# Kernel optimization log

Measured on AMD Instinct MI355X. Metric: run time of the kernel, lower is better.

Reference implementation:

```python
import jax, jax.numpy as jnp
import numpy as np

N_QUBITS = 15
N_LAYERS = 4
N_GATES = 3   # gate_pool = [rx, ry, rz]
N_CLASSES = 4
K_PRIME = 4
BATCH = 64
TAU = 1.0


def _gate_bank(theta):
    """theta: float[...]. Returns complex64[..., 3, 2, 2] = stacked RX/RY/RZ(theta)."""
    th = theta.astype(jnp.float32)
    c = jnp.cos(th / 2).astype(jnp.complex64)
    s = jnp.sin(th / 2).astype(jnp.complex64)
    z = jnp.zeros_like(c)
    isn = 1j * s
    rx = jnp.stack([jnp.stack([c, -isn], -1), jnp.stack([-isn, c], -1)], -2)
    ry = jnp.stack([jnp.stack([c, -s], -1), jnp.stack([s, c], -1)], -2)
    e_m = jnp.exp(-0.5j * th).astype(jnp.complex64)
    e_p = jnp.exp(0.5j * th).astype(jnp.complex64)
    rz = jnp.stack([jnp.stack([e_m, z], -1), jnp.stack([z, e_p], -1)], -2)
    return jnp.stack([rx, ry, rz], -3)


def _apply_1q(state, U, q):
    """Apply a single-qubit gate to qubit q. state: [B] + [2]*n. U: [2,2] or [B,2,2]."""
    s = jnp.moveaxis(state, 1 + q, -1)
    if U.ndim == 2:
        s = jnp.einsum('ij,b...j->b...i', U, s)
    else:
        s = jnp.einsum('bij,b...j->b...i', U, s)
    return jnp.moveaxis(s, -1, 1 + q)


def _apply_cnot(state, c, t):
    """CNOT with control c, target t on state [B] + [2]*n."""
    c0 = jax.lax.slice_in_dim(state, 0, 1, axis=1 + c)
    c1 = jax.lax.slice_in_dim(state, 1, 2, axis=1 + c)
    c1 = jnp.flip(c1, axis=1 + t)
    return jnp.concatenate([c0, c1], axis=1 + c)


def setup_inputs() -> dict:
    key = jax.random.key(0)
    k1, k2, k3, k4, k5 = jax.random.split(key, 5)
    x = jax.random.uniform(k1, (BATCH, N_QUBITS), jnp.float32) * np.float32(np.pi)
    P = jax.random.normal(k2, (N_LAYERS, N_QUBITS, 1, K_PRIME), jnp.float32)
    Q = jax.random.normal(k3, (N_LAYERS, N_QUBITS, K_PRIME, N_GATES), jnp.float32)
    rotation_params = jax.random.uniform(k4, (N_LAYERS * N_QUBITS,), jnp.float32) * np.float32(2 * np.pi)
    u = jax.random.uniform(k5, (N_LAYERS, N_QUBITS, N_GATES), jnp.float32, 1e-6, 1.0 - 1e-6)
    gumbel_noise = -jnp.log(-jnp.log(u))
    return {"x": x, "P": P, "Q": Q, "rotation_params": rotation_params,
            "gumbel_noise": gumbel_noise}


def reference(x, P, Q, rotation_params, gumbel_noise):
    B = x.shape[0]
    n = N_QUBITS
    # architecture logits = (P @ Q).squeeze(2)  -> [L, n, G]
    logits = (P @ Q).squeeze(2)
    # hard gumbel-softmax with straight-through estimator
    y_soft = jax.nn.softmax((logits + gumbel_noise) / TAU, axis=-1)
    y_hard = jax.nn.one_hot(jnp.argmax(y_soft, axis=-1), N_GATES, dtype=y_soft.dtype)
    onehot = y_hard + y_soft - jax.lax.stop_gradient(y_soft)  # [L, n, G]

    # |0...0> initial state, shape [B] + [2]*n
    state = jnp.zeros((B,) + (2,) * n, jnp.complex64).at[(slice(None),) + (0,) * n].set(1.0)

    # angle-encode data: RY(x_q) on qubit q
    enc = _gate_bank(x)[..., 1, :, :]  # [B, n, 2, 2] (RY bank)
    for q in range(n):
        state = _apply_1q(state, enc[:, q], q)

    # per-layer selected parametrized rotations, mixed by one-hot (hard fwd, soft grad)
    theta = rotation_params.reshape(N_LAYERS, n)
    banks = _gate_bank(theta)  # [L, n, 3, 2, 2]
    U = jnp.einsum('lqg,lqgij->lqij', onehot.astype(jnp.complex64), banks)
    for l in range(N_LAYERS):
        for q in range(n):
            state = _apply_1q(state, U[l, q], q)
        for q in range(n):  # entangling CNOT ring
            state = _apply_cnot(state, q, (q + 1) % n)

    amps = state.reshape(B, -1)
    probs = amps.real ** 2 + amps.imag ** 2  # [B, 2^n]
    M = probs.shape[1]
    # aggregate contiguous basis-state blocks into class probabilities
    return probs.reshape(B, N_CLASSES, M // N_CLASSES).sum(-1)
```

## Files before the change

### kernel.cpp

```cpp
#include <hip/hip_runtime.h>

#define BLOCK 512
#define NAMPS 64
#define CHUNK 32

struct St {
  float2 a0,a1,a2,a3,a4,a5,a6,a7,a8,a9,a10,a11,a12,a13,a14,a15,
         a16,a17,a18,a19,a20,a21,a22,a23,a24,a25,a26,a27,a28,a29,a30,a31,
         a32,a33,a34,a35,a36,a37,a38,a39,a40,a41,a42,a43,a44,a45,a46,a47,
         a48,a49,a50,a51,a52,a53,a54,a55,a56,a57,a58,a59,a60,a61,a62,a63;
  template<int I> __device__ __forceinline__ float2& g(){
    if constexpr (I==0) return a0;   else if constexpr (I==1) return a1;
    else if constexpr (I==2) return a2;   else if constexpr (I==3) return a3;
    else if constexpr (I==4) return a4;   else if constexpr (I==5) return a5;
    else if constexpr (I==6) return a6;   else if constexpr (I==7) return a7;
    else if constexpr (I==8) return a8;   else if constexpr (I==9) return a9;
    else if constexpr (I==10) return a10; else if constexpr (I==11) return a11;
    else if constexpr (I==12) return a12; else if constexpr (I==13) return a13;
    else if constexpr (I==14) return a14; else if constexpr (I==15) return a15;
    else if constexpr (I==16) return a16; else if constexpr (I==17) return a17;
    else if constexpr (I==18) return a18; else if constexpr (I==19) return a19;
    else if constexpr (I==20) return a20; else if constexpr (I==21) return a21;
    else if constexpr (I==22) return a22; else if constexpr (I==23) return a23;
    else if constexpr (I==24) return a24; else if constexpr (I==25) return a25;
    else if constexpr (I==26) return a26; else if constexpr (I==27) return a27;
    else if constexpr (I==28) return a28; else if constexpr (I==29) return a29;
    else if constexpr (I==30) return a30; else if constexpr (I==31) return a31;
    else if constexpr (I==32) return a32; else if constexpr (I==33) return a33;
    else if constexpr (I==34) return a34; else if constexpr (I==35) return a35;
    else if constexpr (I==36) return a36; else if constexpr (I==37) return a37;
    else if constexpr (I==38) return a38; else if constexpr (I==39) return a39;
    else if constexpr (I==40) return a40; else if constexpr (I==41) return a41;
    else if constexpr (I==42) return a42; else if constexpr (I==43) return a43;
    else if constexpr (I==44) return a44; else if constexpr (I==45) return a45;
    else if constexpr (I==46) return a46; else if constexpr (I==47) return a47;
    else if constexpr (I==48) return a48; else if constexpr (I==49) return a49;
    else if constexpr (I==50) return a50; else if constexpr (I==51) return a51;
    else if constexpr (I==52) return a52; else if constexpr (I==53) return a53;
    else if constexpr (I==54) return a54; else if constexpr (I==55) return a55;
    else if constexpr (I==56) return a56; else if constexpr (I==57) return a57;
    else if constexpr (I==58) return a58; else if constexpr (I==59) return a59;
    else if constexpr (I==60) return a60; else if constexpr (I==61) return a61;
    else if constexpr (I==62) return a62; else return a63;
  }
};

__device__ __forceinline__ float2 cmadd2(float2 u, float2 a, float2 v, float2 b){
  return make_float2(u.x*a.x - u.y*a.y + v.x*b.x - v.y*b.y,
                     u.x*a.y + u.y*a.x + v.x*b.y + v.y*b.x);
}


template<int BL, int K>
__device__ __forceinline__ void rot_local_impl(St& st, float2 u00, float2 u01, float2 u10, float2 u11){
  if constexpr (K < NAMPS){
    if constexpr (!(K & (1<<BL))){
      constexpr int K1 = K | (1<<BL);
      float2 x0 = st.g<K>(), x1 = st.g<K1>();
      st.g<K>()  = cmadd2(u00, x0, u01, x1);
      st.g<K1>() = cmadd2(u10, x0, u11, x1);
    }
    rot_local_impl<BL, K+1>(st, u00, u01, u10, u11);
  }
}
template<int BL>
__device__ __forceinline__ void rot_local(St& st, const float* u){
  float2 u00 = make_float2(u[0],u[1]), u01 = make_float2(u[2],u[3]);
  float2 u10 = make_float2(u[4],u[5]), u11 = make_float2(u[6],u[7]);
  rot_local_impl<BL, 0>(st, u00, u01, u10, u11);
}

template<int LB, int K>
__device__ __forceinline__ void rot_lane_impl(St& st, float2 ua, float2 ub){
  if constexpr (K < NAMPS){
    float2 A = st.g<K>();
    float2 p;
    p.x = __shfl_xor(A.x, 1<<LB, 64);
    p.y = __shfl_xor(A.y, 1<<LB, 64);
    st.g<K>() = cmadd2(ua, A, ub, p);
    rot_lane_impl<LB, K+1>(st, ua, ub);
  }
}
template<int LB>
__device__ __forceinline__ void rot_lane(St& st, const float* u, int lane){
  const int bit = (lane >> LB) & 1;
  float2 u00 = make_float2(u[0],u[1]), u01 = make_float2(u[2],u[3]);
  float2 u10 = make_float2(u[4],u[5]), u11 = make_float2(u[6],u[7]);
  float2 ua = bit ? u11 : u00;
  float2 ub = bit ? u10 : u01;
  rot_lane_impl<LB, 0>(st, ua, ub);
}

template<int Base, int K>
__device__ __forceinline__ void stw_impl(St& st, float2* xbuf, int t){
  if constexpr (K < CHUNK){
    xbuf[K*BLOCK + t] = st.g<Base + K>();
    stw_impl<Base, K+1>(st, xbuf, t);
  }
}
template<int Base, int K>
__device__ __forceinline__ void ldr_rot_impl(St& st, const float2* xbuf, int partner, float2 ua, float2 ub){
  if constexpr (K < CHUNK){
    float2 p = xbuf[K*BLOCK + partner];
    float2 A = st.g<Base + K>();
    st.g<Base + K>() = cmadd2(ua, A, ub, p);
    ldr_rot_impl<Base, K+1>(st, xbuf, partner, ua, ub);
  }
}
template<int Base, int K>
__device__ __forceinline__ void ldr_mov_impl(St& st, const float2* xbuf, int src){
  if constexpr (K < CHUNK){
    st.g<Base + K>() = xbuf[K*BLOCK + src];
    ldr_mov_impl<Base, K+1>(st, xbuf, src);
  }
}

template<int WB>
__device__ __forceinline__ void rot_wave(St& st, const float* u, int t, float2* xbuf){
  const int partner = t ^ (64 << WB);
  const int bit = (t >> (6 + WB)) & 1;
  float2 u00 = make_float2(u[0],u[1]), u01 = make_float2(u[2],u[3]);
  float2 u10 = make_float2(u[4],u[5]), u11 = make_float2(u[6],u[7]);
  float2 ua = bit ? u11 : u00;
  float2 ub = bit ? u10 : u01;
  __syncthreads();
  stw_impl<0, 0>(st, xbuf, t);
  __syncthreads();
  ldr_rot_impl<0, 0>(st, xbuf, partner, ua, ub);
  __syncthreads();
  stw_impl<32, 0>(st, xbuf, t);
  __syncthreads();
  ldr_rot_impl<32, 0>(st, xbuf, partner, ua, ub);
}

__device__ __forceinline__ void cnot_wavechain(St& st, int t, float2* xbuf){
  const int wave = t >> 6, lane = t & 63;
  const int src = ((wave ^ ((wave >> 1) & 3)) << 6) | lane;
  __syncthreads();
  stw_impl<0, 0>(st, xbuf, t);
  __syncthreads();
  ldr_mov_impl<0, 0>(st, xbuf, src);
  __syncthreads();
  stw_impl<32, 0>(st, xbuf, t);
  __syncthreads();
  ldr_mov_impl<32, 0>(st, xbuf, src);
}

template<int K>
__device__ __forceinline__ void lanechain_impl(St& st, int src){
  if constexpr (K < NAMPS){
    float2 A = st.g<K>();
    float2 p;
    p.x = __shfl(A.x, src, 64);
    p.y = __shfl(A.y, src, 64);
    st.g<K>() = p;
    lanechain_impl<K+1>(st, src);
  }
}
__device__ __forceinline__ void cnot_lanechain(St& st, int t){
  const int lane = t & 63;
  const int w0 = (t >> 6) & 1;
  const int src = lane ^ ((lane >> 1) & 31) ^ (w0 << 5);
  lanechain_impl<0>(st, src);
}

template<int K>
__device__ __forceinline__ void q8_impl(St& st, bool ctrl){
  if constexpr (K < 32){
    constexpr int K1 = K | 32;
    float2 x0 = st.g<K>(), x1 = st.g<K1>();
    st.g<K>()  = ctrl ? x1 : x0;
    st.g<K1>() = ctrl ? x0 : x1;
    q8_impl<K+1>(st, ctrl);
  }
}

template<int K>
__device__ __forceinline__ void ripple_impl(St& dst, St& src){
  if constexpr (K < NAMPS){
    dst.g<K>() = src.g<K ^ ((K>>1) & 31)>();
    ripple_impl<K+1>(dst, src);
  }
}

template<int K>
__device__ __forceinline__ void q14_w_impl(St& st, float2* xbuf, int t){
  if constexpr (K < 32){
    xbuf[K*BLOCK + t] = st.g<2*K + 1>();
    q14_w_impl<K+1>(st, xbuf, t);
  }
}
template<int K>
__device__ __forceinline__ void q14_r_impl(St& st, const float2* xbuf, int partner){
  if constexpr (K < 32){
    st.g<2*K + 1>() = xbuf[K*BLOCK + partner];
    q14_r_impl<K+1>(st, xbuf, partner);
  }
}
__device__ __forceinline__ void cnot_q14(St& st, int t, float2* xbuf){
  const int partner = t ^ 256;
  __syncthreads();
  q14_w_impl<0>(st, xbuf, t);
  __syncthreads();
  q14_r_impl<0>(st, xbuf, partner);
}

template<int K>
__device__ __forceinline__ void init_impl(St& st, float hp,
                                          float lc0, float lc1, float lc2, float lc3, float lc4, float lc5,
                                          float ls0, float ls1, float ls2, float ls3, float ls4, float ls5){
  if constexpr (K < NAMPS){
    float v = hp;
    v *= (K & 32) ? ls5 : lc5;
    v *= (K & 16) ? ls4 : lc4;
    v *= (K & 8)  ? ls3 : lc3;
    v *= (K & 4)  ? ls2 : lc2;
    v *= (K & 2)  ? ls1 : lc1;
    v *= (K & 1)  ? ls0 : lc0;
    st.g<K>() = make_float2(v, 0.f);
    init_impl<K+1>(st, hp, lc0,lc1,lc2,lc3,lc4,lc5, ls0,ls1,ls2,ls3,ls4,ls5);
  }
}

template<int K>
__device__ __forceinline__ float sumsq_impl(St& st, float acc){
  if constexpr (K < NAMPS){
    float2 A = st.g<K>();
    return sumsq_impl<K+1>(st, acc + A.x*A.x + A.y*A.y);
  } else return acc;
}

__global__ __attribute__((amdgpu_flat_work_group_size(BLOCK,BLOCK), amdgpu_waves_per_eu(2,2)))
void qdarts_kernel(const float* __restrict__ x,
                   const float* __restrict__ P,
                   const float* __restrict__ Q,
                   const float* __restrict__ rot,
                   const float* __restrict__ gn,
                   float* __restrict__ out)
{
  __shared__ float2 xbuf[CHUNK * BLOCK];
  __shared__ float  umat[60 * 8];
  __shared__ float  part[8];

  const int t    = threadIdx.x;
  const int b    = blockIdx.x;
  const int lane = t & 63;
  const int wave = t >> 6;

  if (t < 60){
    const int idx = t;
    const float* Pv = P  + idx*4;
    const float* Qv = Q  + idx*12;
    const float* gv = gn + idx*3;
    int g = 0; float best = -1e30f;
    #pragma unroll
    for (int j = 0; j < 3; j++){
      float lg = Pv[0]*Qv[0*3+j] + Pv[1]*Qv[1*3+j] + Pv[2]*Qv[2*3+j] + Pv[3]*Qv[3*3+j] + gv[j];
      if (lg > best){ best = lg; g = j; }
    }
    const float half = rot[idx] * 0.5f;
    const float c = cosf(half), s = sinf(half);
    float m0,m1,m2,m3,m4,m5,m6,m7;
    if (g == 0){
      m0=c; m1=0.f; m2=0.f; m3=-s; m4=0.f; m5=-s; m6=c; m7=0.f;
    } else if (g == 1){
      m0=c; m1=0.f; m2=-s; m3=0.f; m4=s; m5=0.f; m6=c; m7=0.f;
    } else {
      m0=c; m1=-s; m2=0.f; m3=0.f; m4=0.f; m5=0.f; m6=c; m7=s;
    }
    umat[idx*8+0]=m0; umat[idx*8+1]=m1; umat[idx*8+2]=m2; umat[idx*8+3]=m3;
    umat[idx*8+4]=m4; umat[idx*8+5]=m5; umat[idx*8+6]=m6; umat[idx*8+7]=m7;
  }
  __syncthreads();

  const float* xb = x + b*15;
  float hp = 1.f;
  #pragma unroll
  for (int q = 0; q < 9; q++){
    const float h = xb[q]*0.5f;
    hp *= ((t >> (8-q)) & 1) ? sinf(h) : cosf(h);
  }
  float lc0,lc1,lc2,lc3,lc4,lc5, ls0,ls1,ls2,ls3,ls4,ls5;
  { float h;
    h = xb[14]*0.5f; lc0 = cosf(h); ls0 = sinf(h);
    h = xb[13]*0.5f; lc1 = cosf(h); ls1 = sinf(h);
    h = xb[12]*0.5f; lc2 = cosf(h); ls2 = sinf(h);
    h = xb[11]*0.5f; lc3 = cosf(h); ls3 = sinf(h);
    h = xb[10]*0.5f; lc4 = cosf(h); ls4 = sinf(h);
    h = xb[9] *0.5f; lc5 = cosf(h); ls5 = sinf(h);
  }
  St st;
  init_impl<0>(st, hp, lc0,lc1,lc2,lc3,lc4,lc5, ls0,ls1,ls2,ls3,ls4,ls5);

  for (int l = 0; l < 4; l++){
    const float* U = umat + l*15*8;
    rot_local<5>(st, U + 9*8);
    rot_local<4>(st, U + 10*8);
    rot_local<3>(st, U + 11*8);
    rot_local<2>(st, U + 12*8);
    rot_local<1>(st, U + 13*8);
    rot_local<0>(st, U + 14*8);
    rot_lane<5>(st, U + 3*8, lane);
    rot_lane<4>(st, U + 4*8, lane);
    rot_lane<3>(st, U + 5*8, lane);
    rot_lane<2>(st, U + 6*8, lane);
    rot_lane<1>(st, U + 7*8, lane);
    rot_lane<0>(st, U + 8*8, lane);
    rot_wave<2>(st, U + 0*8, t, xbuf);
    rot_wave<1>(st, U + 1*8, t, xbuf);
    rot_wave<0>(st, U + 2*8, t, xbuf);
    cnot_wavechain(st, t, xbuf);
    cnot_lanechain(st, t);
    q8_impl<0>(st, (bool)(lane & 1));
    { St tmp; ripple_impl<0>(tmp, st); st = tmp; }
    cnot_q14(st, t, xbuf);
  }

  float s = sumsq_impl<0>(st, 0.f);
  #pragma unroll
  for (int off = 32; off > 0; off >>= 1) s += __shfl_down(s, off, 64);
  if (lane == 0) part[wave] = s;
  __syncthreads();
  if (t < 4){
    out[b*4 + t] = part[2*t] + part[2*t+1];
  }
}

extern "C" void kernel_launch(void* const* d_in, const int* in_sizes, int n_in,
                              void* d_out, int out_size, void* d_ws, size_t ws_size,
                              hipStream_t stream) {
  const float* x   = (const float*)d_in[0];
  const float* P   = (const float*)d_in[1];
  const float* Q   = (const float*)d_in[2];
  const float* rot = (const float*)d_in[3];
  const float* gn  = (const float*)d_in[4];
  float* out = (float*)d_out;
  hipLaunchKernelGGL(qdarts_kernel, dim3(64), dim3(BLOCK), 0, stream,
                     x, P, Q, rot, gn, out);
}
```

Measured before the change: 225.8 us.

## Use DPP for low-lane rotations, 128-bit LDS exchanges, fuse q2 rotation with CNOT chain

Measured after the change: 237.6 us. +5.2%, slower.

```diff
diff --git a/kernel.cpp b/kernel.cpp
--- a/kernel.cpp
+++ b/kernel.cpp
@@ -91,32 +91,61 @@
   rot_lane_impl<LB, 0>(st, ua, ub);
 }
 
-template<int Base, int K>
-__device__ __forceinline__ void stw_impl(St& st, float2* xbuf, int t){
-  if constexpr (K < CHUNK){
-    xbuf[K*BLOCK + t] = st.g<Base + K>();
-    stw_impl<Base, K+1>(st, xbuf, t);
-  }
-}
-template<int Base, int K>
-__device__ __forceinline__ void ldr_rot_impl(St& st, const float2* xbuf, int partner, float2 ua, float2 ub){
-  if constexpr (K < CHUNK){
-    float2 p = xbuf[K*BLOCK + partner];
-    float2 A = st.g<Base + K>();
-    st.g<Base + K>() = cmadd2(ua, A, ub, p);
-    ldr_rot_impl<Base, K+1>(st, xbuf, partner, ua, ub);
-  }
-}
-template<int Base, int K>
-__device__ __forceinline__ void ldr_mov_impl(St& st, const float2* xbuf, int src){
-  if constexpr (K < CHUNK){
-    st.g<Base + K>() = xbuf[K*BLOCK + src];
-    ldr_mov_impl<Base, K+1>(st, xbuf, src);
+template<int CTRL>
+__device__ __forceinline__ float dppf(float v){
+  int i = __float_as_int(v);
+  return __int_as_float(__builtin_amdgcn_update_dpp(i, i, CTRL, 0xF, 0xF, false));
+}
+template<int CTRL, int K>
+__device__ __forceinline__ void rot_dpp_impl(St& st, float2 ua, float2 ub){
+  if constexpr (K < NAMPS){
+    float2 A = st.g<K>();
+    float2 p = make_float2(dppf<CTRL>(A.x), dppf<CTRL>(A.y));
+    st.g<K>() = cmadd2(ua, A, ub, p);
+    rot_dpp_impl<CTRL, K+1>(st, ua, ub);
+  }
+}
+template<int LB, int CTRL>
+__device__ __forceinline__ void rot_dpp(St& st, const float* u, int lane){
+  const int bit = (lane >> LB) & 1;
+  float2 u00 = make_float2(u[0],u[1]), u01 = make_float2(u[2],u[3]);
+  float2 u10 = make_float2(u[4],u[5]), u11 = make_float2(u[6],u[7]);
+  float2 ua = bit ? u11 : u00;
+  float2 ub = bit ? u10 : u01;
+  rot_dpp_impl<CTRL, 0>(st, ua, ub);
+}
+
+template<int Base, int K2>
+__device__ __forceinline__ void stw128_impl(St& st, float4* xb4, int t){
+  if constexpr (K2 < 16){
+    float2 a = st.g<Base + 2*K2>(), b = st.g<Base + 2*K2 + 1>();
+    xb4[K2*BLOCK + t] = make_float4(a.x, a.y, b.x, b.y);
+    stw128_impl<Base, K2+1>(st, xb4, t);
+  }
+}
+template<int Base, int K2>
+__device__ __forceinline__ void ldr128_rot_impl(St& st, const float4* xb4, int partner, float2 ua, float2 ub){
+  if constexpr (K2 < 16){
+    float4 p = xb4[K2*BLOCK + partner];
+    float2 A = st.g<Base + 2*K2>(), B = st.g<Base + 2*K2 + 1>();
+    st.g<Base + 2*K2>()     = cmadd2(ua, A, ub, make_float2(p.x, p.y));
+    st.g<Base + 2*K2 + 1>() = cmadd2(ua, B, ub, make_float2(p.z, p.w));
+    ldr128_rot_impl<Base, K2+1>(st, xb4, partner, ua, ub);
+  }
+}
+template<int Base, int K2>
+__device__ __forceinline__ void fread_impl(St& st, const float4* xb4, int s, int s2, float2 ua, float2 ub){
+  if constexpr (K2 < 16){
+    float4 p = xb4[K2*BLOCK + s];
+    float4 q = xb4[K2*BLOCK + s2];
+    st.g<Base + 2*K2>()     = cmadd2(ua, make_float2(p.x,p.y), ub, make_float2(q.x,q.y));
+    st.g<Base + 2*K2 + 1>() = cmadd2(ua, make_float2(p.z,p.w), ub, make_float2(q.z,q.w));
+    fread_impl<Base, K2+1>(st, xb4, s, s2, ua, ub);
   }
 }
 
 template<int WB>
-__device__ __forceinline__ void rot_wave(St& st, const float* u, int t, float2* xbuf){
+__device__ __forceinline__ void rot_wave(St& st, const float* u, int t, float4* xb4){
   const int partner = t ^ (64 << WB);
   const int bit = (t >> (6 + WB)) & 1;
   float2 u00 = make_float2(u[0],u[1]), u01 = make_float2(u[2],u[3]);
@@ -124,26 +153,32 @@
   float2 ua = bit ? u11 : u00;
   float2 ub = bit ? u10 : u01;
   __syncthreads();
-  stw_impl<0, 0>(st, xbuf, t);
-  __syncthreads();
-  ldr_rot_impl<0, 0>(st, xbuf, partner, ua, ub);
-  __syncthreads();
-  stw_impl<32, 0>(st, xbuf, t);
-  __syncthreads();
-  ldr_rot_impl<32, 0>(st, xbuf, partner, ua, ub);
-}
-
-__device__ __forceinline__ void cnot_wavechain(St& st, int t, float2* xbuf){
+  stw128_impl<0, 0>(st, xb4, t);
+  __syncthreads();
+  ldr128_rot_impl<0, 0>(st, xb4, partner, ua, ub);
+  __syncthreads();
+  stw128_impl<32, 0>(st, xb4, t);
+  __syncthreads();
+  ldr128_rot_impl<32, 0>(st, xb4, partner, ua, ub);
+}
+
+__device__ __forceinline__ void rotq2_wavechain(St& st, const float* u, int t, float4* xb4){
   const int wave = t >> 6, lane = t & 63;
-  const int src = ((wave ^ ((wave >> 1) & 3)) << 6) | lane;
-  __syncthreads();
-  stw_impl<0, 0>(st, xbuf, t);
-  __syncthreads();
-  ldr_mov_impl<0, 0>(st, xbuf, src);
-  __syncthreads();
-  stw_impl<32, 0>(st, xbuf, t);
-  __syncthreads();
-  ldr_mov_impl<32, 0>(st, xbuf, src);
+  const int s  = ((wave ^ ((wave >> 1) & 3)) << 6) | lane;
+  const int s2 = s ^ 64;
+  const int sbit = (s >> 6) & 1;
+  float2 u00 = make_float2(u[0],u[1]), u01 = make_float2(u[2],u[3]);
+  float2 u10 = make_float2(u[4],u[5]), u11 = make_float2(u[6],u[7]);
+  float2 ua = sbit ? u11 : u00;
+  float2 ub = sbit ? u10 : u01;
+  __syncthreads();
+  stw128_impl<0, 0>(st, xb4, t);
+  __syncthreads();
+  fread_impl<0, 0>(st, xb4, s, s2, ua, ub);
+  __syncthreads();
+  stw128_impl<32, 0>(st, xb4, t);
+  __syncthreads();
+  fread_impl<32, 0>(st, xb4, s, s2, ua, ub);
 }
 
 template<int K>
@@ -184,25 +219,25 @@
 }
 
 template<int K>
-__device__ __forceinline__ void q14_w_impl(St& st, float2* xbuf, int t){
+__device__ __forceinline__ void q14_w_impl(St& st, float2* xb2, int t){
   if constexpr (K < 32){
-    xbuf[K*BLOCK + t] = st.g<2*K + 1>();
-    q14_w_impl<K+1>(st, xbuf, t);
-  }
-}
-template<int K>
-__device__ __forceinline__ void q14_r_impl(St& st, const float2* xbuf, int partner){
+    xb2[K*BLOCK + t] = st.g<2*K + 1>();
+    q14_w_impl<K+1>(st, xb2, t);
+  }
+}
+template<int K>
+__device__ __forceinline__ void q14_r_impl(St& st, const float2* xb2, int partner){
   if constexpr (K < 32){
-    st.g<2*K + 1>() = xbuf[K*BLOCK + partner];
-    q14_r_impl<K+1>(st, xbuf, partner);
-  }
-}
-__device__ __forceinline__ void cnot_q14(St& st, int t, float2* xbuf){
+    st.g<2*K + 1>() = xb2[K*BLOCK + partner];
+    q14_r_impl<K+1>(st, xb2, partner);
+  }
+}
+__device__ __forceinline__ void cnot_q14(St& st, int t, float2* xb2){
   const int partner = t ^ 256;
   __syncthreads();
-  q14_w_impl<0>(st, xbuf, t);
-  __syncthreads();
-  q14_r_impl<0>(st, xbuf, partner);
+  q14_w_impl<0>(st, xb2, t);
+  __syncthreads();
+  q14_r_impl<0>(st, xb2, partner);
 }
 
 template<int K>
@@ -221,7 +256,6 @@
     init_impl<K+1>(st, hp, lc0,lc1,lc2,lc3,lc4,lc5, ls0,ls1,ls2,ls3,ls4,ls5);
   }
 }
-
 template<int K>
 __device__ __forceinline__ float sumsq_impl(St& st, float acc){
   if constexpr (K < NAMPS){
@@ -238,9 +272,10 @@
                    const float* __restrict__ gn,
                    float* __restrict__ out)
 {
-  __shared__ float2 xbuf[CHUNK * BLOCK];
+  __shared__ float4 xb4[16 * BLOCK];
   __shared__ float  umat[60 * 8];
   __shared__ float  part[8];
+  float2* xb2 = reinterpret_cast<float2*>(xb4);
 
   const int t    = threadIdx.x;
   const int b    = blockIdx.x;
@@ -304,16 +339,15 @@
     rot_lane<4>(st, U + 4*8, lane);
     rot_lane<3>(st, U + 5*8, lane);
     rot_lane<2>(st, U + 6*8, lane);
-    rot_lane<1>(st, U + 7*8, lane);
-    rot_lane<0>(st, U + 8*8, lane);
-    rot_wave<2>(st, U + 0*8, t, xbuf);
-    rot_wave<1>(st, U + 1*8, t, xbuf);
-    rot_wave<0>(st, U + 2*8, t, xbuf);
-    cnot_wavechain(st, t, xbuf);
+    rot_dpp<1, 0x4E>(st, U + 7*8, lane);
+    rot_dpp<0, 0xB1>(st, U + 8*8, lane);
+    rot_wave<2>(st, U + 0*8, t, xb4);
+    rot_wave<1>(st, U + 1*8, t, xb4);
+    rotq2_wavechain(st, U + 2*8, t, xb4);
     cnot_lanechain(st, t);
     q8_impl<0>(st, (bool)(lane & 1));
     { St tmp; ripple_impl<0>(tmp, st); st = tmp; }
-    cnot_q14(st, t, xbuf);
+    cnot_q14(st, t, xb2);
   }
 
   float s = sumsq_impl<0>(st, 0.f);
```
